# Performance work log

Hardware: AMD Instinct MI355X
Metric: run time of the kernel (lower is better)

## Reference

```python
import jax, jax.numpy as jnp
import numpy as np

N = 100_000   # num_nodes
E = 1_600_000 # num edges (avg degree 16)
D = 128       # embedding_dim
L = 3         # num_layers


def setup_inputs() -> dict:
    key = jax.random.key(0)
    k1, k2, k3 = jax.random.split(key, 3)
    row = jax.random.randint(k1, (E,), 0, N, dtype=jnp.int32)
    # ensure every node appears at least once as a target so degree > 0
    col = jnp.concatenate([
        jnp.arange(N, dtype=jnp.int32),
        jax.random.randint(k2, (E - N,), 0, N, dtype=jnp.int32),
    ])
    edge_index = jnp.stack([row, col])  # [2, E]
    emb = jax.random.normal(k3, (N, D), dtype=jnp.float32) * 0.1  # nn.Embedding init std=0.1
    return {"emb": emb, "edge_index": edge_index}


def _lightgcn_layer(x, row, col):
    # degree over target nodes (col), as in degree(col)
    deg = jax.ops.segment_sum(jnp.ones_like(col, dtype=x.dtype), col, num_segments=N)
    deg_inv_sqrt = jnp.where(deg > 0, jax.lax.rsqrt(deg), jnp.array(0.0, x.dtype))
    norm = deg_inv_sqrt[row] * deg_inv_sqrt[col]          # [E]
    msg = norm[:, None] * x[row]                          # gather + scale, [E, D]
    return jax.ops.segment_sum(msg, col, num_segments=N)  # scatter-add, [N, D]


def reference(emb, edge_index):
    row, col = edge_index[0], edge_index[1]
    x = emb
    acc = x
    for _ in range(L):  # small fixed layer count
        x = _lightgcn_layer(x, row, col)
        acc = acc + x
    # mean over the L+1 layer-wise embeddings (stack(...).mean(0) without materializing the stack)
    return acc / jnp.array(L + 1, emb.dtype)
```

## Files before the change

### kernel.cpp

```cpp
#include <hip/hip_runtime.h>
#include <hip/hip_fp16.h>
#include <hip/hip_fp8.h>

#define NN 100000
#define DD 128
#define NSUB 128
#define SUBN 782
#define PCAP_REC 14000
#define CSTRIDE 16000
#define PCNT_PAD 16
#define FP8_SCALE 64.0f
#define FP8_INV (1.0f / 64.0f)

typedef float v2f __attribute__((ext_vector_type(2)));

#if __has_builtin(__builtin_amdgcn_cvt_pk_f32_fp8) && __has_builtin(__builtin_amdgcn_cvt_pk_fp8_f32)
#define HW_FP8 1
#else
#define HW_FP8 0
#endif

__device__ __forceinline__ v2f dec2(int w, int hi) {
#if HW_FP8
    return hi ? __builtin_amdgcn_cvt_pk_f32_fp8(w, 1)
              : __builtin_amdgcn_cvt_pk_f32_fp8(w, 0);
#else
    unsigned short hw = hi ? (unsigned short)((unsigned)w >> 16) : (unsigned short)(w & 0xffff);
    __half2_raw r = __hip_cvt_fp8x2_to_halfraw2((__hip_fp8x2_storage_t)hw, __HIP_E4M3);
    __half2 h; *reinterpret_cast<__half2_raw*>(&h) = r;
    float2 f = __half22float2(h);
    v2f o; o.x = f.x; o.y = f.y; return o;
#endif
}
__device__ __forceinline__ int enc2(float a, float b, int old, int hi) {
#if HW_FP8
    return hi ? __builtin_amdgcn_cvt_pk_fp8_f32(a, b, old, 1)
              : __builtin_amdgcn_cvt_pk_fp8_f32(a, b, old, 0);
#else
    unsigned short p = __hip_cvt_float2_to_fp8x2(make_float2(a, b), __HIP_SATFINITE, __HIP_E4M3);
    return hi ? ((old & 0xffff) | ((int)p << 16)) : ((old & ~0xffff) | (int)p);
#endif
}

__global__ __launch_bounds__(256) void part_kernel(
    const int* __restrict__ row, const int* __restrict__ col,
    int* __restrict__ pcnt, int* __restrict__ part, int E) {
    __shared__ int bcnt[NSUB], gbase[NSUB];
    if (threadIdx.x < NSUB) bcnt[threadIdx.x] = 0;
    __syncthreads();
    int beg = blockIdx.x * 1024;
    int subv[4], pv[4], recv[4];
    #pragma unroll
    for (int e = 0; e < 4; ++e) {
        int i = beg + e * 256 + (int)threadIdx.x;
        subv[e] = -1;
        if (i < E) {
            int c = col[i];
            int r = row[i];
            int sb = (int)((unsigned)c / SUBN);
            subv[e] = sb;
            recv[e] = (r << 10) | (c - sb * SUBN);
            pv[e] = atomicAdd(&bcnt[sb], 1);
        }
    }
    __syncthreads();
    if (threadIdx.x < NSUB)
        gbase[threadIdx.x] = atomicAdd(&pcnt[threadIdx.x * PCNT_PAD], bcnt[threadIdx.x]);
    __syncthreads();
    #pragma unroll
    for (int e = 0; e < 4; ++e) {
        if (subv[e] >= 0) {
            int p = gbase[subv[e]] + pv[e];
            if (p < PCAP_REC)
                part[(size_t)subv[e] * PCAP_REC + p] = recv[e];
        }
    }
}

__global__ __launch_bounds__(1024) void build_kernel(
    const int* __restrict__ pcnt, const int* __restrict__ part,
    int* __restrict__ cnt, int* __restrict__ offs, int* __restrict__ csr) {
    __shared__ int lcnt[SUBN];
    __shared__ int lofs[SUBN];
    __shared__ int lpos[SUBN];
    __shared__ int sh[1024];
    int s = blockIdx.x;
    int base_node = s * SUBN;
    int tid = threadIdx.x;
    for (int t = tid; t < SUBN; t += 1024) { lcnt[t] = 0; lpos[t] = 0; }
    __syncthreads();
    int M = min(pcnt[s * PCNT_PAD], PCAP_REC);
    const int* __restrict__ p = part + (size_t)s * PCAP_REC;
    for (int t = tid; t < M; t += 1024)
        atomicAdd(&lcnt[p[t] & 1023], 1);
    __syncthreads();
    int v = (tid < SUBN) ? ((lcnt[tid] + 3) & ~3) : 0;
    sh[tid] = v;
    __syncthreads();
    for (int d = 1; d < 1024; d <<= 1) {
        int add = (tid >= d) ? sh[tid - d] : 0;
        __syncthreads();
        sh[tid] += add;
        __syncthreads();
    }
    if (tid < SUBN) {
        int excl = sh[tid] - v;
        lofs[tid] = excl;
        int node = base_node + tid;
        if (node < NN) {
            offs[node] = s * CSTRIDE + excl;
            cnt[node] = lcnt[tid];
        }
    }
    __syncthreads();
    int* __restrict__ dst = csr + (size_t)s * CSTRIDE;
    for (int t = tid; t < M; t += 1024) {
        int rec = p[t];
        int local = rec & 1023;
        int pos = lofs[local] + atomicAdd(&lpos[local], 1);
        if (pos < CSTRIDE) dst[pos] = rec >> 10;
    }
}

__global__ void conv_kernel(const float* __restrict__ emb, const int* __restrict__ cnt,
                            unsigned int* __restrict__ x0_8) {
    int i = blockIdx.x * blockDim.x + threadIdx.x;
    if (i < NN * DD / 4) {
        int n = cnt[i >> 5];
        float s = n > 0 ? FP8_SCALE * rsqrtf((float)n) : 0.0f;
        float4 v = ((const float4*)emb)[i];
        int w = enc2(s * v.x, s * v.y, 0, 0);
        w = enc2(s * v.z, s * v.w, w, 1);
        x0_8[i] = (unsigned)w;
    }
}

template<int MODE>
__global__ __launch_bounds__(256) void gather_kernel(
    const unsigned char* __restrict__ x8,
    const int* __restrict__ cnt,
    const int* __restrict__ offs,
    const int* __restrict__ csr,
    __half* __restrict__ x16_out,
    unsigned char* __restrict__ x8_out,
    const float* __restrict__ emb,
    const __half* __restrict__ u1p,
    const __half* __restrict__ u2p,
    float* __restrict__ out)
{
    int node = __builtin_amdgcn_readfirstlane(blockIdx.x * 4 + (threadIdx.x >> 6));
    if (node >= NN) return;
    int lane = threadIdx.x & 63;
    int g = lane >> 4;
    int q = lane & 15;

    int n = cnt[node];
    int off = offs[node];
    int srcs = csr[off + lane];

    v2f a0 = {0.f, 0.f}, a1 = {0.f, 0.f}, a2 = {0.f, 0.f}, a3 = {0.f, 0.f};

    int nn = n < 64 ? n : 64;
    int T = (nn + 3) >> 2;
    for (int t = 0; t < T; ++t) {
        int j = (t << 2) | g;
        int s = __shfl(srcs, j);
        if (j < nn) {
            int2 raw = *(const int2*)(x8 + ((size_t)s << 7) + (q << 3));
            a0 += dec2(raw.x, 0);
            a1 += dec2(raw.x, 1);
            a2 += dec2(raw.y, 0);
            a3 += dec2(raw.y, 1);
        }
    }
    for (int j = 64 + g; j < n; j += 4) {
        int s = csr[off + j];
        int2 raw = *(const int2*)(x8 + ((size_t)s << 7) + (q << 3));
        a0 += dec2(raw.x, 0);
        a1 += dec2(raw.x, 1);
        a2 += dec2(raw.y, 0);
        a3 += dec2(raw.y, 1);
    }
    float av[8] = {a0.x, a0.y, a1.x, a1.y, a2.x, a2.y, a3.x, a3.y};
    #pragma unroll
    for (int k = 0; k < 8; ++k) {
        av[k] += __shfl_xor(av[k], 16);
        av[k] += __shfl_xor(av[k], 32);
    }

    if (g == 0) {
        float fn = (float)n;
        if (MODE == 0) {
            float inv = n > 0 ? 1.0f / fn : 0.0f;
            float m16 = inv * FP8_INV;
            __half2 h16[4];
            #pragma unroll
            for (int k = 0; k < 4; ++k)
                h16[k] = __float22half2_rn(make_float2(av[2 * k] * m16, av[2 * k + 1] * m16));
            *(int4*)(x16_out + (size_t)node * DD + q * 8) = *(int4*)h16;
            int w0 = enc2(av[0] * inv, av[1] * inv, 0, 0);
            w0 = enc2(av[2] * inv, av[3] * inv, w0, 1);
            int w1 = enc2(av[4] * inv, av[5] * inv, 0, 0);
            w1 = enc2(av[6] * inv, av[7] * inv, w1, 1);
            *(int2*)(x8_out + ((size_t)node << 7) + (q << 3)) = make_int2(w0, w1);
        } else {
            float d = n > 0 ? rsqrtf(fn) : 0.0f;
            float rr = n > 0 ? sqrtf(fn) : 0.0f;
            float d64 = d * FP8_INV;
            size_t eo = (size_t)node * DD + q * 8;
            float4 e0 = *(const float4*)(emb + eo);
            float4 e1 = *(const float4*)(emb + eo + 4);
            float e8[8] = {e0.x, e0.y, e0.z, e0.w, e1.x, e1.y, e1.z, e1.w};
            int4 b1 = *(const int4*)(u1p + eo);
            int4 b2 = *(const int4*)(u2p + eo);
            const __half2* h1 = (const __half2*)&b1;
            const __half2* h2v = (const __half2*)&b2;
            float o8[8];
            #pragma unroll
            for (int k = 0; k < 4; ++k) {
                float2 uu1 = __half22float2(h1[k]);
                float2 uu2 = __half22float2(h2v[k]);
                o8[2 * k]     = 0.25f * (e8[2 * k]     + (uu1.x + uu2.x) * rr + d64 * av[2 * k]);
                o8[2 * k + 1] = 0.25f * (e8[2 * k + 1] + (uu1.y + uu2.y) * rr + d64 * av[2 * k + 1]);
            }
            float* dst = out + eo;
            *(float4*)dst       = make_float4(o8[0], o8[1], o8[2], o8[3]);
            *(float4*)(dst + 4) = make_float4(o8[4], o8[5], o8[6], o8[7]);
        }
    }
}


extern "C" void kernel_launch(void* const* d_in, const int* in_sizes, int n_in,
                              void* d_out, int out_size, void* d_ws, size_t ws_size,
                              hipStream_t stream) {
    const float* emb = (const float*)d_in[0];
    const int* ei = (const int*)d_in[1];
    const int E = in_sizes[1] / 2;
    const int* row = ei;
    const int* col = ei + E;
    float* out = (float*)d_out;

    char* w = (char*)d_ws;
    auto align_up = [](size_t v) { return (v + 255) & ~(size_t)255; };
    size_t o = 0;
    int* pcnt = (int*)(w + o);           o = align_up(o + (size_t)NSUB * PCNT_PAD * 4);
    int* cnt  = (int*)(w + o);           o = align_up(o + (size_t)NN * 4);
    int* offs = (int*)(w + o);           o = align_up(o + (size_t)NN * 4);
    int* csr  = (int*)(w + o);           o = align_up(o + (size_t)NSUB * CSTRIDE * 4);
    char* upx = w + o;                   o = align_up(o + (size_t)NN * DD);
    int* part = (int*)upx;
    unsigned char* xs2_8 = (unsigned char*)upx;
    unsigned char* xs0_8 = (unsigned char*)(w + o); o = align_up(o + (size_t)NN * DD);
    unsigned char* xs1_8 = (unsigned char*)(w + o); o = align_up(o + (size_t)NN * DD);
    __half* xs1_16 = (__half*)(w + o);   o = align_up(o + (size_t)NN * DD * 2);
    __half* xs2_16 = (__half*)(w + o);   o = align_up(o + (size_t)NN * DD * 2);

    hipMemsetAsync(pcnt, 0, (size_t)NSUB * PCNT_PAD * 4, stream);

    part_kernel<<<(E + 1023) / 1024, 256, 0, stream>>>(row, col, pcnt, part, E);
    build_kernel<<<NSUB, 1024, 0, stream>>>(pcnt, part, cnt, offs, csr);
    conv_kernel<<<(NN * DD / 4 + 255) / 256, 256, 0, stream>>>(emb, cnt, (unsigned int*)xs0_8);

    const int lb = (NN * 64) / 256;
    gather_kernel<0><<<lb, 256, 0, stream>>>(xs0_8, cnt, offs, csr, xs1_16, xs1_8,
                                             nullptr, nullptr, nullptr, nullptr);
    gather_kernel<0><<<lb, 256, 0, stream>>>(xs1_8, cnt, offs, csr, xs2_16, xs2_8,
                                             nullptr, nullptr, nullptr, nullptr);
    gather_kernel<1><<<lb, 256, 0, stream>>>(xs2_8, cnt, offs, csr, nullptr, nullptr,
                                             emb, xs1_16, xs2_16, out);
}
```

Baseline: 223.3 us.

## Batch partition work, prequantize embedding to fp16, and use nontemporal stores

The partition kernel now handles 4096 edges per block instead of 1024, so fewer blocks issue global atomics on the partition counters. conv_kernel also writes a pre-scaled fp16 copy of the input embedding, which the final layer reads instead of fp32 emb, halving that read at the cost of an extra 25.6MB write earlier. Output and intermediate stores become nontemporal, the final combine folds the 0.25 factor into precomputed scalars, and the CSR preload is masked by degree. Rounding the original embedding term to fp16 adds a little precision loss to the output.

```diff
diff --git a/kernel.cpp b/kernel.cpp
--- a/kernel.cpp
+++ b/kernel.cpp
@@ -9,10 +9,14 @@
 #define PCAP_REC 14000
 #define CSTRIDE 16000
 #define PCNT_PAD 16
+#define PEB 4096
 #define FP8_SCALE 64.0f
 #define FP8_INV (1.0f / 64.0f)
 
 typedef float v2f __attribute__((ext_vector_type(2)));
+typedef int   v2i __attribute__((ext_vector_type(2)));
+typedef int   v4i __attribute__((ext_vector_type(4)));
+typedef float v4f __attribute__((ext_vector_type(4)));
 
 #if __has_builtin(__builtin_amdgcn_cvt_pk_f32_fp8) && __has_builtin(__builtin_amdgcn_cvt_pk_fp8_f32)
 #define HW_FP8 1
@@ -48,10 +52,10 @@
     __shared__ int bcnt[NSUB], gbase[NSUB];
     if (threadIdx.x < NSUB) bcnt[threadIdx.x] = 0;
     __syncthreads();
-    int beg = blockIdx.x * 1024;
-    int subv[4], pv[4], recv[4];
+    int beg = blockIdx.x * PEB;
+    int subv[16], pv[16], recv[16];
     #pragma unroll
-    for (int e = 0; e < 4; ++e) {
+    for (int e = 0; e < 16; ++e) {
         int i = beg + e * 256 + (int)threadIdx.x;
         subv[e] = -1;
         if (i < E) {
@@ -68,7 +72,7 @@
         gbase[threadIdx.x] = atomicAdd(&pcnt[threadIdx.x * PCNT_PAD], bcnt[threadIdx.x]);
     __syncthreads();
     #pragma unroll
-    for (int e = 0; e < 4; ++e) {
+    for (int e = 0; e < 16; ++e) {
         if (subv[e] >= 0) {
             int p = gbase[subv[e]] + pv[e];
             if (p < PCAP_REC)
@@ -123,7 +127,7 @@
 }
 
 __global__ void conv_kernel(const float* __restrict__ emb, const int* __restrict__ cnt,
-                            unsigned int* __restrict__ x0_8) {
+                            unsigned int* __restrict__ x0_8, __half* __restrict__ embq) {
     int i = blockIdx.x * blockDim.x + threadIdx.x;
     if (i < NN * DD / 4) {
         int n = cnt[i >> 5];
@@ -132,6 +136,10 @@
         int w = enc2(s * v.x, s * v.y, 0, 0);
         w = enc2(s * v.z, s * v.w, w, 1);
         x0_8[i] = (unsigned)w;
+        __half2 q[2];
+        q[0] = __float22half2_rn(make_float2(0.25f * v.x, 0.25f * v.y));
+        q[1] = __float22half2_rn(make_float2(0.25f * v.z, 0.25f * v.w));
+        __builtin_nontemporal_store(*(v2i*)q, (v2i*)(embq + (size_t)i * 4));
     }
 }
 
@@ -143,7 +151,7 @@
     const int* __restrict__ csr,
     __half* __restrict__ x16_out,
     unsigned char* __restrict__ x8_out,
-    const float* __restrict__ emb,
+    const __half* __restrict__ embq,
     const __half* __restrict__ u1p,
     const __half* __restrict__ u2p,
     float* __restrict__ out)
@@ -156,7 +164,7 @@
 
     int n = cnt[node];
     int off = offs[node];
-    int srcs = csr[off + lane];
+    int srcs = (lane < n) ? csr[off + lane] : 0;
 
     v2f a0 = {0.f, 0.f}, a1 = {0.f, 0.f}, a2 = {0.f, 0.f}, a3 = {0.f, 0.f};
 
@@ -197,35 +205,37 @@
             #pragma unroll
             for (int k = 0; k < 4; ++k)
                 h16[k] = __float22half2_rn(make_float2(av[2 * k] * m16, av[2 * k + 1] * m16));
-            *(int4*)(x16_out + (size_t)node * DD + q * 8) = *(int4*)h16;
+            __builtin_nontemporal_store(*(v4i*)h16, (v4i*)(x16_out + (size_t)node * DD + q * 8));
             int w0 = enc2(av[0] * inv, av[1] * inv, 0, 0);
             w0 = enc2(av[2] * inv, av[3] * inv, w0, 1);
             int w1 = enc2(av[4] * inv, av[5] * inv, 0, 0);
             w1 = enc2(av[6] * inv, av[7] * inv, w1, 1);
-            *(int2*)(x8_out + ((size_t)node << 7) + (q << 3)) = make_int2(w0, w1);
+            v2i w01; w01.x = w0; w01.y = w1;
+            __builtin_nontemporal_store(w01, (v2i*)(x8_out + ((size_t)node << 7) + (q << 3)));
         } else {
-            float d = n > 0 ? rsqrtf(fn) : 0.0f;
-            float rr = n > 0 ? sqrtf(fn) : 0.0f;
-            float d64 = d * FP8_INV;
+            float rr4 = n > 0 ? 0.25f * sqrtf(fn) : 0.0f;
+            float d644 = n > 0 ? 0.25f * FP8_INV * rsqrtf(fn) : 0.0f;
             size_t eo = (size_t)node * DD + q * 8;
-            float4 e0 = *(const float4*)(emb + eo);
-            float4 e1 = *(const float4*)(emb + eo + 4);
-            float e8[8] = {e0.x, e0.y, e0.z, e0.w, e1.x, e1.y, e1.z, e1.w};
+            int4 bq = *(const int4*)(embq + eo);
             int4 b1 = *(const int4*)(u1p + eo);
             int4 b2 = *(const int4*)(u2p + eo);
+            const __half2* hq = (const __half2*)&bq;
             const __half2* h1 = (const __half2*)&b1;
             const __half2* h2v = (const __half2*)&b2;
             float o8[8];
             #pragma unroll
             for (int k = 0; k < 4; ++k) {
+                float2 eq = __half22float2(hq[k]);
                 float2 uu1 = __half22float2(h1[k]);
                 float2 uu2 = __half22float2(h2v[k]);
-                o8[2 * k]     = 0.25f * (e8[2 * k]     + (uu1.x + uu2.x) * rr + d64 * av[2 * k]);
-                o8[2 * k + 1] = 0.25f * (e8[2 * k + 1] + (uu1.y + uu2.y) * rr + d64 * av[2 * k + 1]);
+                o8[2 * k]     = eq.x + (uu1.x + uu2.x) * rr4 + d644 * av[2 * k];
+                o8[2 * k + 1] = eq.y + (uu1.y + uu2.y) * rr4 + d644 * av[2 * k + 1];
             }
             float* dst = out + eo;
-            *(float4*)dst       = make_float4(o8[0], o8[1], o8[2], o8[3]);
-            *(float4*)(dst + 4) = make_float4(o8[4], o8[5], o8[6], o8[7]);
+            v4f lo; lo.x = o8[0]; lo.y = o8[1]; lo.z = o8[2]; lo.w = o8[3];
+            v4f hi; hi.x = o8[4]; hi.y = o8[5]; hi.z = o8[6]; hi.w = o8[7];
+            __builtin_nontemporal_store(lo, (v4f*)dst);
+            __builtin_nontemporal_store(hi, (v4f*)(dst + 4));
         }
     }
 }
@@ -255,12 +265,13 @@
     unsigned char* xs1_8 = (unsigned char*)(w + o); o = align_up(o + (size_t)NN * DD);
     __half* xs1_16 = (__half*)(w + o);   o = align_up(o + (size_t)NN * DD * 2);
     __half* xs2_16 = (__half*)(w + o);   o = align_up(o + (size_t)NN * DD * 2);
+    __half* embq   = (__half*)(w + o);   o = align_up(o + (size_t)NN * DD * 2);
 
     hipMemsetAsync(pcnt, 0, (size_t)NSUB * PCNT_PAD * 4, stream);
 
-    part_kernel<<<(E + 1023) / 1024, 256, 0, stream>>>(row, col, pcnt, part, E);
+    part_kernel<<<(E + PEB - 1) / PEB, 256, 0, stream>>>(row, col, pcnt, part, E);
     build_kernel<<<NSUB, 1024, 0, stream>>>(pcnt, part, cnt, offs, csr);
-    conv_kernel<<<(NN * DD / 4 + 255) / 256, 256, 0, stream>>>(emb, cnt, (unsigned int*)xs0_8);
+    conv_kernel<<<(NN * DD / 4 + 255) / 256, 256, 0, stream>>>(emb, cnt, (unsigned int*)xs0_8, embq);
 
     const int lb = (NN * 64) / 256;
     gather_kernel<0><<<lb, 256, 0, stream>>>(xs0_8, cnt, offs, csr, xs1_16, xs1_8,
@@ -268,5 +279,5 @@
     gather_kernel<0><<<lb, 256, 0, stream>>>(xs1_8, cnt, offs, csr, xs2_16, xs2_8,
                                              nullptr, nullptr, nullptr, nullptr);
     gather_kernel<1><<<lb, 256, 0, stream>>>(xs2_8, cnt, offs, csr, nullptr, nullptr,
-                                             emb, xs1_16, xs2_16, out);
-}
+                                             embq, xs1_16, xs2_16, out);
+}
```

Result: no change. 220.7 us (-1.1%).
